# Performance work log

Hardware: AMD Instinct MI355X
Metric: run time of the kernel (lower is better)

## Reference

```python
import jax, jax.numpy as jnp
import numpy as np

E = 128          # number of bot groups (envs)
NB = 256         # bots per group
DQ = DK = DV = 256
D = DQ + DK + DV # 768
COM_RANGE = 15.0
KV_NOISE = 0.05
NEG = -1000000.0


def setup_inputs() -> dict:
    key = jax.random.key(0)
    k1, k2, k3, k4 = jax.random.split(key, 4)
    N = E * NB
    qkv = jax.random.normal(k1, (N, D), dtype=jnp.float32)
    # audibility mask: [N_total, n_per_group]; mask[bot_slice] -> [n, n] per group
    mask = jax.random.bernoulli(k2, 0.9, (N, NB))
    # 2D positions in a 30x30 arena so ~half of pairs fall within com_range
    bot_pos = jax.random.uniform(k3, (N, 2), dtype=jnp.float32, minval=0.0, maxval=30.0)
    # kv noise: zero on the q part [:K_DIM], gaussian(std=kv_noise) on k,v part
    noise = jnp.concatenate(
        [jnp.zeros((N, DQ), jnp.float32),
         KV_NOISE * jax.random.normal(k4, (N, DK + DV), dtype=jnp.float32)],
        axis=-1)
    s = jnp.float32(0.0)  # nn.Parameter init
    return {"qkv": qkv, "mask": mask, "bot_pos": bot_pos, "noise": noise, "s": s}


def reference(qkv, mask, bot_pos, noise, s):
    # noise injection on k,v channels (noise is zero on q channels)
    qkv = qkv + noise
    scale_s = jnp.abs(s) + 1.0

    # all bot groups are equal-sized -> batch the per-slice loop as [E, NB, ...]
    qkv_g = qkv.reshape(E, NB, D)
    q = qkv_g[..., :DQ] * scale_s
    k = qkv_g[..., DQ:DQ + DK]
    v = qkv_g[..., DQ + DK:]

    # pairwise-distance range mask per group
    pos = bot_pos.reshape(E, NB, 2)
    bdiff = pos[:, None, :, :] - pos[:, :, None, :]          # [E, NB, NB, 2]
    range_mask = jnp.linalg.norm(bdiff, axis=-1) < COM_RANGE  # [E, NB, NB]

    audible = mask.reshape(E, NB, NB) & range_mask            # [E, NB, NB]

    # SDPA with additive mask (torch adds -1e6 where masked)
    scores = jnp.einsum('eqd,ekd->eqk', q, k) / jnp.sqrt(jnp.float32(DK))
    scores = scores + jnp.where(audible, 0.0, NEG)
    attn = jax.nn.softmax(scores, axis=-1)
    x = jnp.einsum('eqk,ekd->eqd', attn, v)                   # [E, NB, DV]

    # zero out bots that hear nobody
    x = x * audible.any(axis=-1, keepdims=True)
    return x.reshape(E * NB, DV)
```

## Files before the change

kernel.cpp:

```cpp
#include <hip/hip_runtime.h>
#include <hip/hip_bf16.h>
#include <stdint.h>


#define EE   128
#define NBB  256
#define DDIM 768
#define NEGV (-1000000.0f)

typedef __attribute__((ext_vector_type(8))) short short8;
typedef __attribute__((ext_vector_type(4))) float f32x4;

__device__ __forceinline__ unsigned short f2bf(float f){
  union { float f; unsigned u; } v; v.f = f;
  return (unsigned short)((v.u + 0x7FFFu + ((v.u >> 16) & 1u)) >> 16);
}
__device__ __forceinline__ unsigned short cvt1(float f){
  __hip_bfloat16 h = __float2bfloat16(f);
  unsigned short u; __builtin_memcpy(&u, &h, 2); return u;
}
__device__ __forceinline__ unsigned pk2(float lo, float hi){
  return (unsigned)cvt1(lo) | ((unsigned)cvt1(hi) << 16);
}

__device__ __forceinline__ void swap32(unsigned &a, unsigned &b){
#if __has_builtin(__builtin_amdgcn_permlane32_swap)
  auto r = __builtin_amdgcn_permlane32_swap(a, b, false, false);
  a = r[0]; b = r[1];
#else
  const int up = threadIdx.x & 32;
  const unsigned ax = __shfl_xor(a, 32), bx = __shfl_xor(b, 32);
  const unsigned na = up ? bx : a, nb = up ? b : ax;
  a = na; b = nb;
#endif
}
__device__ __forceinline__ void swap16(unsigned &a, unsigned &b){
#if __has_builtin(__builtin_amdgcn_permlane16_swap)
  auto r = __builtin_amdgcn_permlane16_swap(a, b, false, false);
  a = r[0]; b = r[1];
#else
  const int odd = threadIdx.x & 16;
  const unsigned ax = __shfl_xor(a, 16), bx = __shfl_xor(b, 16);
  const unsigned na = odd ? bx : a, nb = odd ? b : ax;
  a = na; b = nb;
#endif
}

__device__ __forceinline__ void gload16(const void* g, void* l){
  __builtin_amdgcn_global_load_lds((const __attribute__((address_space(1))) unsigned*)g,
                                   (__attribute__((address_space(3))) unsigned*)l, 16, 0, 0);
}
__device__ __forceinline__ void gstage(const unsigned short* __restrict__ base,
                                       unsigned short* __restrict__ buf,
                                       int wave, int lane){
  #pragma unroll
  for(int i = 0; i < 8; ++i){
    const int lrow = wave*16 + i*2 + (lane >> 5);
    const int col  = ((lane & 31) * 8) ^ ((lrow & 7) << 3);
    gload16(base + (size_t)lrow * 256 + col, buf + (wave*16 + i*2) * 256);
  }
}

__global__ void k_prep(const float* __restrict__ qkv, const float* __restrict__ noise,
                       unsigned short* __restrict__ Vt, unsigned short* __restrict__ Kb){
  __shared__ unsigned short tile[64 * 66];
  if(blockIdx.x < 2048){
    const int b = blockIdx.x;
    const int e = b >> 4, t4 = b & 15;
    const int k0 = (t4 >> 2) << 6, d0 = (t4 & 3) << 6;
    const int u = threadIdx.x & 15, r = threadIdx.x >> 4;
    #pragma unroll
    for(int i = 0; i < 4; ++i){
      const int kl = r + (i << 4);
      const size_t off = ((size_t)(e*NBB + k0 + kl)) * DDIM + 512 + d0 + (u << 2);
      f32x4 v  = *(const f32x4*)(qkv   + off);
      f32x4 nz = *(const f32x4*)(noise + off);
      const int base = kl * 66 + (u << 2);
      tile[base+0] = f2bf(v[0]+nz[0]); tile[base+1] = f2bf(v[1]+nz[1]);
      tile[base+2] = f2bf(v[2]+nz[2]); tile[base+3] = f2bf(v[3]+nz[3]);
    }
    __syncthreads();
    #pragma unroll
    for(int i = 0; i < 4; ++i){
      const int dl = r + (i << 4);
      unsigned short o0 = tile[(u*4+0)*66 + dl];
      unsigned short o1 = tile[(u*4+1)*66 + dl];
      unsigned short o2 = tile[(u*4+2)*66 + dl];
      unsigned short o3 = tile[(u*4+3)*66 + dl];
      *(ushort4*)(Vt + ((size_t)(e*NBB + d0 + dl)) * NBB + k0 + (u << 2)) =
          make_ushort4(o0, o1, o2, o3);
    }
  } else {
    const int b2 = blockIdx.x - 2048;
    const int n  = b2*8 + (threadIdx.x >> 5);
    const int col = (threadIdx.x & 31) * 8;
    const size_t off = (size_t)n * DDIM + 256 + col;
    f32x4 a0 = *(const f32x4*)(qkv + off),   a1 = *(const f32x4*)(qkv + off + 4);
    f32x4 n0 = *(const f32x4*)(noise + off), n1 = *(const f32x4*)(noise + off + 4);
    short8 o;
    o[0]=f2bf(a0[0]+n0[0]); o[1]=f2bf(a0[1]+n0[1]); o[2]=f2bf(a0[2]+n0[2]); o[3]=f2bf(a0[3]+n0[3]);
    o[4]=f2bf(a1[0]+n1[0]); o[5]=f2bf(a1[1]+n1[1]); o[6]=f2bf(a1[2]+n1[2]); o[7]=f2bf(a1[3]+n1[3]);
    *(short8*)(Kb + (size_t)n * 256 + col) = o;
  }
}

__launch_bounds__(256, 2)
__global__ void k_attn(const float* __restrict__ qkv, const float* __restrict__ sp,
                       const unsigned char* __restrict__ m8, const int* __restrict__ m32,
                       const float* __restrict__ pos,
                       const unsigned short* __restrict__ Vt,
                       const unsigned short* __restrict__ Kb,
                       float* __restrict__ out){
  extern __shared__ unsigned char smem[];
  unsigned short* buf0 = (unsigned short*)smem;
  unsigned short* buf1 = (unsigned short*)(smem + 32768);
  unsigned*       audL = (unsigned*)(smem + 65536);
  unsigned long long* audW = (unsigned long long*)(smem + 65536);
  float*          posx = (float*)(smem + 67584);
  float*          posy = (float*)(smem + 68608);

  const int bid = blockIdx.x;
  const int e   = ((bid & 7) << 4) + (bid >> 5);
  const int qq  = (bid >> 3) & 3;
  const int tid  = threadIdx.x;
  const int wave = tid >> 6;
  const int lane = tid & 63;
  const int g    = lane >> 4;
  const int u    = lane & 15;
  const int q0   = qq * 64 + wave * 16;
  const size_t ebase = (size_t)e * NBB;

  {
    const float2 p = *(const float2*)(pos + (ebase + tid) * 2);
    posx[tid] = p.x; posy[tid] = p.y;
  }
  const unsigned probe = ((const unsigned*)m32)[tid & 63];
  const int isInt = !__any(probe > 1u);
  __syncthreads();

  gstage(Kb + ebase * 256, buf0, wave, lane);

  {
    const int rowBase = qq*64 + wave*16;
    #pragma unroll
    for(int ch = 0; ch < 4; ++ch){
      const float kx = posx[ch*64 + lane];
      const float ky = posy[ch*64 + lane];
      #pragma unroll
      for(int rr = 0; rr < 16; ++rr){
        const float qx = posx[rowBase + rr];
        const float qy = posy[rowBase + rr];
        const size_t moff = (ebase + rowBase + rr) * NBB + ch*64 + lane;
        const int mk = isInt ? m32[moff] : (int)m8[moff];
        const float dx = kx - qx, dy = ky - qy;
        const float d2 = __fadd_rn(__fmul_rn(dx, dx), __fmul_rn(dy, dy));
        const unsigned long long b = __ballot((mk != 0) && (sqrtf(d2) < 15.0f));
        if(lane == 0) audW[(wave*16 + rr)*4 + ch] = b;
      }
    }
  }

  const float scale = fabsf(sp[0]) + 1.0f;
  short8 qf[8];
  {
    const float* qrow = qkv + (ebase + q0 + u) * DDIM;
    #pragma unroll
    for(int dk = 0; dk < 8; ++dk){
      f32x4 a = *(const f32x4*)(qrow + dk*32 + g*8);
      f32x4 b = *(const f32x4*)(qrow + dk*32 + g*8 + 4);
      short8 f;
      f[0]=cvt1(a[0]*scale); f[1]=cvt1(a[1]*scale); f[2]=cvt1(a[2]*scale); f[3]=cvt1(a[3]*scale);
      f[4]=cvt1(b[0]*scale); f[5]=cvt1(b[1]*scale); f[6]=cvt1(b[2]*scale); f[7]=cvt1(b[3]*scale);
      qf[dk] = f;
    }
  }

  const f32x4 zero4 = {0.f, 0.f, 0.f, 0.f};
  f32x4 acc[16];
  #pragma unroll
  for(int nt = 0; nt < 16; ++nt) acc[nt] = zero4;

  __syncthreads();

  #pragma unroll
  for(int kq = 0; kq < 4; ++kq){
    unsigned short* cur = (kq & 1) ? buf1 : buf0;
    unsigned short* nxt = (kq & 1) ? buf0 : buf1;
    if(kq < 3) gstage(Kb + (ebase + (size_t)(kq+1) * 64) * 256, nxt, wave, lane);
    else       gstage(Vt + ebase * 256, nxt, wave, lane);
    #pragma unroll
    for(int nth = 0; nth < 4; ++nth){
      const unsigned short* kr = cur + (nth*16 + u) * 256;
      const int sw = (u & 7) << 3;
      #pragma unroll
      for(int dk = 0; dk < 8; ++dk){
        short8 kb = *(const short8*)(kr + ((dk*32 + g*8) ^ sw));
        acc[kq*4 + nth] = __builtin_amdgcn_mfma_f32_16x16x32_bf16(kb, qf[dk], acc[kq*4 + nth], 0, 0, 0);
      }
    }
    if(kq < 3) __syncthreads();
  }

  unsigned wmask[8];
  {
    const unsigned* arow = audL + (wave*16 + u) * 8;
    #pragma unroll
    for(int j = 0; j < 8; ++j) wmask[j] = arow[j];
  }
  const unsigned anyw = wmask[0]|wmask[1]|wmask[2]|wmask[3]|wmask[4]|wmask[5]|wmask[6]|wmask[7];
  const unsigned long long rowsAny = __ballot(anyw != 0u);

  float m0=-3.0e38f, m1=-3.0e38f, m2=-3.0e38f, m3=-3.0e38f;
  #pragma unroll
  for(int nt = 0; nt < 16; ++nt){
    const unsigned wv = wmask[nt >> 1] >> (((nt & 1) << 4) + g*4);
    f32x4 s = acc[nt];
    s[0] = s[0]*0.0625f + ((wv      & 1u) ? 0.0f : NEGV);
    s[1] = s[1]*0.0625f + (((wv>>1) & 1u) ? 0.0f : NEGV);
    s[2] = s[2]*0.0625f + (((wv>>2) & 1u) ? 0.0f : NEGV);
    s[3] = s[3]*0.0625f + (((wv>>3) & 1u) ? 0.0f : NEGV);
    acc[nt] = s;
    m0 = fmaxf(m0, s[0]); m1 = fmaxf(m1, s[1]);
    m2 = fmaxf(m2, s[2]); m3 = fmaxf(m3, s[3]);
  }
  float mx = fmaxf(fmaxf(m0, m1), fmaxf(m2, m3));
  mx = fmaxf(mx, __shfl_xor(mx, 16));
  mx = fmaxf(mx, __shfl_xor(mx, 32));
  float s0=0.f, s1=0.f, s2=0.f, s3=0.f;
  #pragma unroll
  for(int nt = 0; nt < 16; ++nt){
    f32x4 p = acc[nt];
    p[0] = __expf(p[0] - mx); p[1] = __expf(p[1] - mx);
    p[2] = __expf(p[2] - mx); p[3] = __expf(p[3] - mx);
    acc[nt] = p;
    s0 += p[0]; s1 += p[1]; s2 += p[2]; s3 += p[3];
  }
  float ssum = (s0 + s1) + (s2 + s3);
  ssum += __shfl_xor(ssum, 16);
  ssum += __shfl_xor(ssum, 32);
  const float inv = 1.0f / ssum;

  short8 pa[8];
  #pragma unroll
  for(int kt = 0; kt < 8; ++kt){
    unsigned cE = pk2(acc[2*kt][0]*inv,   acc[2*kt][1]*inv);
    unsigned dE = pk2(acc[2*kt][2]*inv,   acc[2*kt][3]*inv);
    unsigned cO = pk2(acc[2*kt+1][0]*inv, acc[2*kt+1][1]*inv);
    unsigned dO = pk2(acc[2*kt+1][2]*inv, acc[2*kt+1][3]*inv);
    swap32(cE, cO); swap16(cE, cO);
    swap32(dE, dO); swap16(dE, dO);
    union { short8 s; unsigned w[4]; } pk;
    pk.w[0] = cE; pk.w[1] = dE; pk.w[2] = cO; pk.w[3] = dO;
    pa[kt] = pk.s;
  }

  __syncthreads();

  #pragma unroll
  for(int dqt = 0; dqt < 4; ++dqt){
    unsigned short* cur = (dqt & 1) ? buf1 : buf0;
    unsigned short* nxt = (dqt & 1) ? buf0 : buf1;
    if(dqt < 3) gstage(Vt + (ebase + (size_t)(dqt+1) * 64) * 256, nxt, wave, lane);
    f32x4 xacc[4];
    #pragma unroll
    for(int dt = 0; dt < 4; ++dt) xacc[dt] = zero4;
    #pragma unroll
    for(int dt = 0; dt < 4; ++dt){
      const unsigned short* vr = cur + (dt*16 + u) * 256;
      const int sw = (u & 7) << 3;
      #pragma unroll
      for(int kt = 0; kt < 8; ++kt){
        short8 bv = *(const short8*)(vr + ((kt*32 + g*8) ^ sw));
        xacc[dt] = __builtin_amdgcn_mfma_f32_16x16x32_bf16(pa[kt], bv, xacc[dt], 0, 0, 0);
      }
    }
    #pragma unroll
    for(int r = 0; r < 4; ++r){
      const float zf = ((rowsAny >> (g*4 + r)) & 1ull) ? 1.0f : 0.0f;
      float* orow = out + (ebase + q0 + g*4 + r) * 256 + dqt*64;
      #pragma unroll
      for(int dt = 0; dt < 4; ++dt)
        orow[dt*16 + u] = xacc[dt][r] * zf;
    }
    if(dqt < 3) __syncthreads();
  }
}

extern "C" void kernel_launch(void* const* d_in, const int* in_sizes, int n_in,
                              void* d_out, int out_size, void* d_ws, size_t ws_size,
                              hipStream_t stream){
  (void)in_sizes; (void)n_in; (void)out_size; (void)ws_size;
  const float* qkv   = (const float*)d_in[0];
  const void*  mask  = d_in[1];
  const float* pos   = (const float*)d_in[2];
  const float* noise = (const float*)d_in[3];
  const float* sp    = (const float*)d_in[4];

  unsigned short* Vt = (unsigned short*)d_ws;
  unsigned short* Kb = (unsigned short*)((unsigned char*)d_ws + 16777216);
  float* outp = (float*)d_out;

  k_prep<<<6144, 256, 0, stream>>>(qkv, noise, Vt, Kb);

  hipFuncSetAttribute((const void*)k_attn, hipFuncAttributeMaxDynamicSharedMemorySize, 69632);
  k_attn<<<512, 256, 69632, stream>>>(qkv, sp,
                                      (const unsigned char*)mask, (const int*)mask,
                                      pos, Vt, Kb, outp);
}
```

Measured before the change: 80.92 us.

## Compute audibility bitmask per thread with vector loads, interleaved with QK MFMA

Replaces the per-row ballot loop for the audibility mask with a layout where each thread builds two 32-bit words from int4 vector loads of the mask and does the distance tests itself. The work is split into four chunks spread across the first three iterations of the K-tile loop, so the mask loads overlap the MFMA score computation. The words go to shared memory before the softmax reads them. This adds register pressure and unrolled code size, and the byte path keeps its original staggering across chunks.

```diff
diff --git a/kernel.cpp b/kernel.cpp
--- a/kernel.cpp
+++ b/kernel.cpp
@@ -115,7 +115,6 @@
   unsigned short* buf0 = (unsigned short*)smem;
   unsigned short* buf1 = (unsigned short*)(smem + 32768);
   unsigned*       audL = (unsigned*)(smem + 65536);
-  unsigned long long* audW = (unsigned long long*)(smem + 65536);
   float*          posx = (float*)(smem + 67584);
   float*          posy = (float*)(smem + 68608);
 
@@ -140,25 +139,56 @@
 
   gstage(Kb + ebase * 256, buf0, wave, lane);
 
-  {
-    const int rowBase = qq*64 + wave*16;
-    #pragma unroll
-    for(int ch = 0; ch < 4; ++ch){
-      const float kx = posx[ch*64 + lane];
-      const float ky = posy[ch*64 + lane];
-      #pragma unroll
-      for(int rr = 0; rr < 16; ++rr){
-        const float qx = posx[rowBase + rr];
-        const float qy = posy[rowBase + rr];
-        const size_t moff = (ebase + rowBase + rr) * NBB + ch*64 + lane;
-        const int mk = isInt ? m32[moff] : (int)m8[moff];
-        const float dx = kx - qx, dy = ky - qy;
-        const float d2 = __fadd_rn(__fmul_rn(dx, dx), __fmul_rn(dy, dy));
-        const unsigned long long b = __ballot((mk != 0) && (sqrtf(d2) < 15.0f));
-        if(lane == 0) audW[(wave*16 + rr)*4 + ch] = b;
-      }
-    }
-  }
+  const int row0 = tid >> 3,        j0 = tid & 7;
+  const int row1 = (tid + 256) >> 3, j1 = tid & 7;
+  const float qx0 = posx[qq*64 + row0], qy0 = posy[qq*64 + row0];
+  const float qx1 = posx[qq*64 + row1], qy1 = posy[qq*64 + row1];
+  const size_t mb0 = (ebase + qq*64 + row0) * NBB + j0 * 32;
+  const size_t mb1 = (ebase + qq*64 + row1) * NBB + j1 * 32;
+  unsigned wd0 = 0u, wd1 = 0u;
+
+  #define AUD_INT_HALF(ii, jv, qxv, qyv, mbv, wdv)                              \
+    {                                                                           \
+      const int blk = ((ii) + (jv)) & 7;                                        \
+      const int4 mv = *(const int4*)(m32 + (mbv) + blk * 4);                    \
+      const int mvals[4] = {mv.x, mv.y, mv.z, mv.w};                            \
+      _Pragma("unroll")                                                         \
+      for(int jj = 0; jj < 4; ++jj){                                            \
+        const int kk = blk * 4 + jj;                                            \
+        const int k  = (jv) * 32 + kk;                                          \
+        const float dx = posx[k] - (qxv), dy = posy[k] - (qyv);                 \
+        const float d2 = __fadd_rn(__fmul_rn(dx, dx), __fmul_rn(dy, dy));       \
+        if((mvals[jj] != 0) && (sqrtf(d2) < 15.0f)) (wdv) |= 1u << kk;          \
+      }                                                                         \
+    }
+  #define AUD_BYTE_HALF(i, jv, qxv, qyv, mbv, wdv)                              \
+    {                                                                           \
+      const int4 mv = *(const int4*)(m8 + (mbv) + (i) * 16);                    \
+      const int mvals[4] = {mv.x, mv.y, mv.z, mv.w};                            \
+      _Pragma("unroll")                                                         \
+      for(int jt = 0; jt < 4; ++jt){                                            \
+        const int jj = (jt + (jv)) & 3;                                         \
+        _Pragma("unroll")                                                       \
+        for(int b = 0; b < 4; ++b){                                             \
+          const int kk = (i) * 16 + jj * 4 + b;                                 \
+          const int k  = (jv) * 32 + kk;                                        \
+          const float dx = posx[k] - (qxv), dy = posy[k] - (qyv);               \
+          const float d2 = __fadd_rn(__fmul_rn(dx, dx), __fmul_rn(dy, dy));     \
+          if((((unsigned)mvals[jj] >> (8 * b)) & 0xFFu) && (sqrtf(d2) < 15.0f)) \
+            (wdv) |= 1u << kk;                                                  \
+        }                                                                       \
+      }                                                                         \
+    }
+  #define AUD_CHUNK(C)                                                          \
+    if(isInt){                                                                  \
+      AUD_INT_HALF(2*(C),   j0, qx0, qy0, mb0, wd0)                             \
+      AUD_INT_HALF(2*(C)+1, j0, qx0, qy0, mb0, wd0)                             \
+      AUD_INT_HALF(2*(C),   j1, qx1, qy1, mb1, wd1)                             \
+      AUD_INT_HALF(2*(C)+1, j1, qx1, qy1, mb1, wd1)                             \
+    } else if((C) < 2){                                                         \
+      AUD_BYTE_HALF((C), j0, qx0, qy0, mb0, wd0)                                \
+      AUD_BYTE_HALF((C), j1, qx1, qy1, mb1, wd1)                                \
+    }
 
   const float scale = fabsf(sp[0]) + 1.0f;
   short8 qf[8];
@@ -175,6 +205,8 @@
     }
   }
 
+  AUD_CHUNK(0)
+
   const f32x4 zero4 = {0.f, 0.f, 0.f, 0.f};
   f32x4 acc[16];
   #pragma unroll
@@ -188,6 +220,9 @@
     unsigned short* nxt = (kq & 1) ? buf0 : buf1;
     if(kq < 3) gstage(Kb + (ebase + (size_t)(kq+1) * 64) * 256, nxt, wave, lane);
     else       gstage(Vt + ebase * 256, nxt, wave, lane);
+    if(kq == 0){ AUD_CHUNK(1) }
+    if(kq == 1){ AUD_CHUNK(2) }
+    if(kq == 2){ AUD_CHUNK(3) audL[tid] = wd0; audL[tid + 256] = wd1; }
     #pragma unroll
     for(int nth = 0; nth < 4; ++nth){
       const unsigned short* kr = cur + (nth*16 + u) * 256;
```

Measured after the change: 69.45 us. 1.17x faster.
